# Optimization experiments

Hardware: AMD Instinct MI355X
Metric: run time of the kernel (lower is better)

Reference implementation:

```python
import jax, jax.numpy as jnp
import numpy as np

B, S, H = 8, 4096, 2048
E, F, K = 32, 128, 2
UTIL_BONUS = 0.1
CAP_PENALTY = 0.1


def setup_inputs() -> dict:
    key = jax.random.key(0)
    ks = jax.random.split(key, 4)
    hidden = jax.random.normal(ks[0], (B, S, H), dtype=jnp.float32)
    router_w = 0.02 * jax.random.normal(ks[1], (E, H), dtype=jnp.float32)
    router_b = jnp.zeros((E,), dtype=jnp.float32)
    w1 = 0.02 * jax.random.normal(ks[2], (E, F, H), dtype=jnp.float32)
    b1 = jnp.zeros((E, F), dtype=jnp.float32)
    w2 = 0.02 * jax.random.normal(ks[3], (E, H, F), dtype=jnp.float32)
    b2 = jnp.zeros((E, H), dtype=jnp.float32)
    activation_counts = jnp.zeros((E,), dtype=jnp.float32)
    expert_drift = jnp.zeros((E,), dtype=jnp.float32)
    return {"hidden": hidden, "router_w": router_w, "router_b": router_b,
            "w1": w1, "b1": b1, "w2": w2, "b2": b2,
            "activation_counts": activation_counts, "expert_drift": expert_drift}


def reference(hidden, router_w, router_b, w1, b1, w2, b2, activation_counts, expert_drift):
    # --- router with usage bonus / capacity penalty (buffers are zero at init) ---
    pooled = hidden.mean(axis=1)                      # [B, H]
    base_logits = pooled @ router_w.T + router_b      # [B, E]
    total = activation_counts.sum()
    usage = activation_counts / jnp.maximum(total, 1e-8)
    bonus = jnp.where(total > 0.0, UTIL_BONUS * (1.0 - usage), jnp.zeros_like(usage))
    usage_norm = activation_counts / jnp.maximum(activation_counts.max(), 1e-8)
    drift_norm = expert_drift / jnp.maximum(expert_drift.max(), 1e-8)
    penalty = CAP_PENALTY * 0.5 * (usage_norm + drift_norm)
    logits = base_logits + bonus[None, :] - penalty[None, :]
    router_probs = jax.nn.softmax(logits, axis=-1)    # [B, E]

    topk_probs, topk_idx = jax.lax.top_k(router_probs, K)  # [B, K]
    topk_probs = topk_probs / jnp.maximum(topk_probs.sum(axis=-1, keepdims=True), 1e-8)

    # --- gather selected expert weights and apply to the full sequence ---
    W1 = w1[topk_idx]   # [B, K, F, H]
    B1 = b1[topk_idx]   # [B, K, F]
    W2 = w2[topk_idx]   # [B, K, H, F]
    B2 = b2[topk_idx]   # [B, K, H]

    h1 = jnp.einsum('bsh,bkfh->bksf', hidden, W1) + B1[:, :, None, :]
    h1 = jax.nn.gelu(h1, approximate=False)           # torch nn.GELU default = exact erf
    out = jnp.einsum('bksf,bkhf->bksh', h1, W2) + B2[:, :, None, :]
    delta = jnp.einsum('bk,bksh->bsh', topk_probs, out)  # weighted combine
    return delta, topk_idx, topk_probs, router_probs
```

## Files before the change

### kernel.cpp

```cpp
#include <hip/hip_runtime.h>
#include <hip/hip_bf16.h>

#define BB 8
#define SS 4096
#define HH 2048
#define EE 32
#define FF 128

constexpr size_t DELTA_N = (size_t)BB * SS * HH;
constexpr size_t WELEM = (size_t)EE * FF * HH;
constexpr size_t WBYTES = WELEM * 2;
constexpr size_t HB16_BYTES = (size_t)BB * SS * HH * 2;

typedef short bf16x8 __attribute__((ext_vector_type(8)));
typedef float f32x4 __attribute__((ext_vector_type(4)));
typedef unsigned short u16;
typedef __attribute__((address_space(3))) unsigned char as3u8;
typedef __attribute__((address_space(1))) const unsigned char as1u8;

#define WAITV(N)                                             \
  do {                                                       \
    asm volatile("s_waitcnt vmcnt(" #N ")" ::: "memory");    \
    __builtin_amdgcn_sched_barrier(0);                       \
  } while (0)
#define BARRIER()                                            \
  do {                                                       \
    __builtin_amdgcn_s_barrier();                            \
    __builtin_amdgcn_sched_barrier(0);                       \
  } while (0)

__device__ __forceinline__ u16 f2bfu(float x) {
  unsigned int u = __float_as_uint(x);
  u = (u + 0x7FFFu + ((u >> 16) & 1u)) >> 16;
  return (u16)u;
}

__device__ __forceinline__ unsigned int pk2(float a, float b) {
  union { __hip_bfloat162 h; unsigned int u; } c;
  c.h = __float22bfloat162_rn(make_float2(a, b));
  return c.u;
}

__device__ __forceinline__ bf16x8 pack8(float4 a, float4 b) {
  union { bf16x8 v; unsigned int u[4]; } r;
  r.u[0] = pk2(a.x, a.y);
  r.u[1] = pk2(a.z, a.w);
  r.u[2] = pk2(b.x, b.y);
  r.u[3] = pk2(b.z, b.w);
  return r.v;
}

__device__ __forceinline__ void glds16(const void* g, void* l) {
  __builtin_amdgcn_global_load_lds((as1u8*)g, (as3u8*)l, 16, 0, 0);
}

__global__ void k_zero(float* __restrict__ ws, int n) {
  int i = blockIdx.x * 256 + threadIdx.x;
  if (i < n) ws[i] = 0.0f;
}

__global__ __launch_bounds__(512) void k_poolpack(
    const float* __restrict__ hidden, const float* __restrict__ w1,
    const float* __restrict__ w2, u16* __restrict__ hb16,
    float* __restrict__ psum, u16* __restrict__ w1p, u16* __restrict__ w2p) {
  const int bid = blockIdx.x;
  const int t = threadIdx.x;
  if (bid < 512) {
    const int b  = bid >> 6;
    const int st = bid & 63;
    const float* src = hidden + ((size_t)b * SS + st * 64) * HH + t * 4;
    char* dbase = (char*)hb16 + (size_t)(b * 64 + st) * 262144 + (size_t)(t >> 4) * 8192;
    const int kq = (t & 15) * 8;
    float4 s = make_float4(0.f, 0.f, 0.f, 0.f);
    for (int r = 0; r < 64; ++r) {
      float4 v = *(const float4*)(src + (size_t)r * HH);
      s.x += v.x; s.y += v.y; s.z += v.z; s.w += v.w;
      *(uint2*)(dbase + r * 128 + (kq ^ ((r & 7) << 4))) =
          make_uint2(pk2(v.x, v.y), pk2(v.z, v.w));
    }
    float* pp = psum + (size_t)b * HH + t * 4;
    atomicAdd(pp + 0, s.x);
    atomicAdd(pp + 1, s.y);
    atomicAdd(pp + 2, s.z);
    atomicAdd(pp + 3, s.w);
  } else {
    const int pb = bid - 512;
#pragma unroll 1
    for (int i = 0; i < 8; ++i) {
      unsigned c = (unsigned)pb * 4096u + (unsigned)i * 512u + (unsigned)t;
      const float* src;
      u16* dst;
      if (c < 1048576u) {
        unsigned e = c >> 15, ci = c & 32767u;
        unsigned it = ci >> 10;
        unsigned cb = (ci & 1023u) * 16u;
        unsigned col = cb >> 7;
        unsigned kb = (cb & 127u) ^ ((col & 7u) << 4);
        unsigned k = it * 64u + (kb >> 1);
        src = w1 + ((size_t)(e * 128u + col) * HH + k);
        dst = w1p + (size_t)c * 8;
      } else {
        unsigned c2 = c - 1048576u;
        unsigned e = c2 >> 15, ci = c2 & 32767u;
        unsigned h = ci >> 4;
        unsigned cb = (ci & 15u) * 16u;
        unsigned kb = cb ^ ((h & 7u) << 4);
        unsigned f = kb >> 1;
        src = w2 + ((size_t)(e * 2048u + h) * FF + f);
        dst = w2p + (size_t)c2 * 8;
      }
      float4 a = *(const float4*)src;
      float4 b2v = *(const float4*)(src + 4);
      *(bf16x8*)dst = pack8(a, b2v);
    }
  }
}

__global__ void k_logits(const float* __restrict__ psum, const float* __restrict__ rw,
                         float* __restrict__ logits) {
  int b = blockIdx.x >> 5;
  int e = blockIdx.x & 31;
  int tid = threadIdx.x;
  float acc = 0.0f;
  const float* ps = psum + (size_t)b * HH;
  const float* wr = rw + (size_t)e * HH;
  for (int h = tid; h < HH; h += 256) acc = fmaf(ps[h], wr[h], acc);
  __shared__ float red[256];
  red[tid] = acc;
  __syncthreads();
  for (int w = 128; w > 0; w >>= 1) {
    if (tid < w) red[tid] += red[tid + w];
    __syncthreads();
  }
  if (tid == 0) logits[blockIdx.x] = red[0] * (1.0f / (float)SS);
}

__global__ void k_topk(const float* __restrict__ logits, const float* __restrict__ rb,
                       const float* __restrict__ counts, const float* __restrict__ drift,
                       int* __restrict__ sel, float* __restrict__ pscale,
                       float* __restrict__ out) {
  int t = threadIdx.x;
  int b = t >> 5, e = t & 31;
  float total = 0.0f, cmax = 0.0f, dmax = 0.0f;
  for (int i = 0; i < EE; ++i) {
    float c = counts[i]; total += c; cmax = fmaxf(cmax, c);
    float d = drift[i];  dmax = fmaxf(dmax, d);
  }
  float cnt = counts[e], dr = drift[e];
  float usage = cnt / fmaxf(total, 1e-8f);
  float bonus = (total > 0.0f) ? 0.1f * (1.0f - usage) : 0.0f;
  float un = cnt / fmaxf(cmax, 1e-8f);
  float dn = dr / fmaxf(dmax, 1e-8f);
  float l = logits[t] + rb[e] + bonus - 0.05f * (un + dn);

  float m = l;
  for (int w = 16; w; w >>= 1) m = fmaxf(m, __shfl_xor(m, w, 32));
  float p = expf(l - m);
  float ssum = p;
  for (int w = 16; w; w >>= 1) ssum += __shfl_xor(ssum, w, 32);
  float prob = p / ssum;
  out[DELTA_N + 32 + t] = prob;

  float v1 = prob; int i1 = e;
  for (int w = 16; w; w >>= 1) {
    float ov = __shfl_xor(v1, w, 32); int oi = __shfl_xor(i1, w, 32);
    if (ov > v1 || (ov == v1 && oi < i1)) { v1 = ov; i1 = oi; }
  }
  float v2 = (e == i1) ? -1.0f : prob; int i2 = e;
  for (int w = 16; w; w >>= 1) {
    float ov = __shfl_xor(v2, w, 32); int oi = __shfl_xor(i2, w, 32);
    if (ov > v2 || (ov == v2 && oi < i2)) { v2 = ov; i2 = oi; }
  }
  if (e == 0) {
    float denom = fmaxf(v1 + v2, 1e-8f);
    float tp0 = v1 / denom, tp1 = v2 / denom;
    sel[b * 2 + 0] = i1;
    sel[b * 2 + 1] = i2;
    pscale[b * 2 + 0] = tp0;
    pscale[b * 2 + 1] = tp1;
    out[DELTA_N + 0 + b * 2 + 0] = (float)i1;
    out[DELTA_N + 0 + b * 2 + 1] = (float)i2;
    out[DELTA_N + 16 + b * 2 + 0] = tp0;
    out[DELTA_N + 16 + b * 2 + 1] = tp1;
  }
}

__global__ __launch_bounds__(512, 4) void k_ffn5(
    const u16* __restrict__ hb16, const float* __restrict__ bs1,
    const float* __restrict__ bs2, const u16* __restrict__ w1p,
    const u16* __restrict__ w2p, const int* __restrict__ sel,
    const float* __restrict__ pscale, float* __restrict__ out) {
  __shared__ __align__(16) char smem[81920];

  const int t    = threadIdx.x;
  const int lane = t & 63;
  const int wv   = t >> 6;
  const int l15  = lane & 15;
  const int lk   = lane >> 4;

  const int bid = blockIdx.x;
  const int b   = bid & 7;
  const int st  = bid >> 3;

  const int e0 = sel[2 * b], e1 = sel[2 * b + 1];
  const float p0 = pscale[2 * b], p1 = pscale[2 * b + 1];

  const int wr = wv >> 2, wc = wv & 3;
  const int RB = wr * 32, CB = wc * 64;

  const char* hsrc = (const char*)hb16 + (size_t)(b * 64 + st) * 262144 + (size_t)t * 16;
  const size_t eB1 = (size_t)((wv < 4) ? e0 : e1) * 524288;
  const char* bsrc = (const char*)w1p + eB1 + (size_t)(wv & 3) * 4096 + (size_t)lane * 16;

  f32x4 zero = {0.f, 0.f, 0.f, 0.f};
  f32x4 acc1[2][4];
#pragma unroll
  for (int i = 0; i < 2; ++i)
#pragma unroll
    for (int j = 0; j < 4; ++j) acc1[i][j] = zero;

  auto STAGE1 = [&](int bb, int j) {
    glds16(hsrc + (size_t)j * 8192, &smem[65536 + bb * 8192 + (size_t)t * 16]);
    const char* s = bsrc + (size_t)j * 16384;
    char* d = &smem[bb * 32768 + wv * 4096 + lane * 16];
#pragma unroll
    for (int r = 0; r < 4; ++r) glds16(s + r * 1024, d + r * 1024);
  };

  STAGE1(0, 0);
  STAGE1(1, 1);

#pragma unroll 1
  for (int j = 0; j < 32; ++j) {
    if (j < 31) { WAITV(5); } else { WAITV(0); }
    BARRIER();
    const int cb = j & 1;
    const char* sa = &smem[65536 + cb * 8192];
    const char* sb = &smem[cb * 32768];
#pragma unroll
    for (int kk = 0; kk < 2; ++kk) {
      bf16x8 af[2], bv[4];
#pragma unroll
      for (int rt = 0; rt < 2; ++rt) {
        int row = RB + rt * 16 + l15;
        af[rt] = *(const bf16x8*)(sa + row * 128 + ((kk * 64 + lk * 16) ^ ((row & 7) << 4)));
      }
#pragma unroll
      for (int ct = 0; ct < 4; ++ct) {
        int col = CB + ct * 16 + l15;
        bv[ct] = *(const bf16x8*)(sb + col * 128 + ((kk * 64 + lk * 16) ^ ((col & 7) << 4)));
      }
#pragma unroll
      for (int rt = 0; rt < 2; ++rt)
#pragma unroll
        for (int ct = 0; ct < 4; ++ct)
          acc1[rt][ct] = __builtin_amdgcn_mfma_f32_16x16x32_bf16(af[rt], bv[ct], acc1[rt][ct], 0, 0, 0);
    }
    BARRIER();
    if (j < 30) STAGE1(j & 1, j + 2);
  }

#pragma unroll
  for (int ct = 0; ct < 4; ++ct) {
    int c = CB + ct * 16 + l15;
    int ec = (c < 128) ? e0 : e1;
    float pc = (c < 128) ? p0 : p1;
    float bias = bs1[ec * FF + (c & 127)];
#pragma unroll
    for (int rt = 0; rt < 2; ++rt)
#pragma unroll
      for (int r = 0; r < 4; ++r) {
        int row = RB + rt * 16 + lk * 4 + r;
        float x = acc1[rt][ct][r] + bias;
        float g = 0.5f * x * (1.0f + erff(x * 0.70710678118654752f));
        *(u16*)&smem[row * 512 + ((c * 2) ^ ((row & 7) << 4))] = f2bfu(pc * g);
      }
  }
  {
    float4 q0 = *(const float4*)(bs2 + (size_t)e0 * HH + t * 4);
    float4 q1 = *(const float4*)(bs2 + (size_t)e1 * HH + t * 4);
    float4 bb;
    bb.x = p0 * q0.x + p1 * q1.x;
    bb.y = p0 * q0.y + p1 * q1.y;
    bb.z = p0 * q0.z + p1 * q1.z;
    bb.w = p0 * q0.w + p1 * q1.w;
    *(float4*)&smem[65536 + t * 16] = bb;
  }
  __syncthreads();

  const int wr2 = wv >> 2, wc2 = wv & 3;
  bf16x8 pa[2][8];
#pragma unroll
  for (int rt = 0; rt < 2; ++rt) {
    int row = wr2 * 32 + rt * 16 + l15;
    unsigned sw = (row & 7) << 4;
#pragma unroll
    for (int ks = 0; ks < 8; ++ks)
      pa[rt][ks] = *(const bf16x8*)&smem[row * 512 + ((ks * 64 + lk * 16) ^ sw)];
  }
  BARRIER();

  const char* wse = (const char*)w2p + (size_t)((wv < 4) ? e0 : e1) * 524288;
  auto STAGE2 = [&](int bb, int n) {
    const char* s = wse + (size_t)(n * 64 + (wv & 3) * 16) * 256 + (size_t)lane * 16;
    char* d = &smem[bb * 32768 + (wv >> 2) * 16384 + (wv & 3) * 4096 + lane * 16];
#pragma unroll
    for (int i = 0; i < 4; ++i) glds16(s + i * 1024, d + i * 1024);
  };
  STAGE2(0, 0);
  STAGE2(1, 1);

  float* obase = out + ((size_t)b * SS + st * 64) * HH;
  const int h64 = wc2 * 16 + l15;

#pragma unroll 1
  for (int n0 = 0; n0 < 32; ++n0) {
    if (n0 == 0) { WAITV(4); }
    else if (n0 == 31) { WAITV(8); }
    else { WAITV(12); }
    BARRIER();
    const char* tb = &smem[(n0 & 1) * 32768];
    float bias = *(const float*)&smem[65536 + (n0 * 64 + h64) * 4];
    f32x4 acc2[2];
    acc2[0] = zero; acc2[1] = zero;
#pragma unroll
    for (int ks = 0; ks < 8; ++ks) {
      bf16x8 bv = *(const bf16x8*)(tb + (ks >> 2) * 16384 + h64 * 256 +
                                   (((ks & 3) * 64 + lk * 16) ^ ((h64 & 7) << 4)));
#pragma unroll
      for (int rt = 0; rt < 2; ++rt)
        acc2[rt] = __builtin_amdgcn_mfma_f32_16x16x32_bf16(pa[rt][ks], bv, acc2[rt], 0, 0, 0);
    }
    BARRIER();
    const int col = n0 * 64 + h64;
#pragma unroll
    for (int rt = 0; rt < 2; ++rt)
#pragma unroll
      for (int r = 0; r < 4; ++r) {
        int row = wr2 * 32 + rt * 16 + lk * 4 + r;
        obase[(size_t)row * HH + col] = acc2[rt][r] + bias;
      }
    if (n0 < 30) STAGE2(n0 & 1, n0 + 2);
  }
}

__global__ void k_pool_logits(const float* __restrict__ hidden,
                              const float* __restrict__ rw,
                              float* __restrict__ logits) {
  const int b  = blockIdx.x >> 6;
  const int hc = (blockIdx.x >> 3) & 7;
  const int sq = blockIdx.x & 7;
  const int t  = threadIdx.x;
  const int tx = t & 63;
  const int qq = t >> 6;
  const int h0 = hc * 256;

  const float* p = hidden + ((size_t)b * SS + sq * 512 + qq * 128) * HH + h0 + tx * 4;
  float4 s = make_float4(0.f, 0.f, 0.f, 0.f);
  for (int i = 0; i < 128; ++i) {
    float4 v = *(const float4*)(p + (size_t)i * HH);
    s.x += v.x; s.y += v.y; s.z += v.z; s.w += v.w;
  }
  __shared__ float ps[4][256];
  __shared__ float pl[256];
  *(float4*)&ps[qq][tx * 4] = s;
  __syncthreads();
  pl[t] = ps[0][t] + ps[1][t] + ps[2][t] + ps[3][t];
  __syncthreads();

  const int e = t >> 3, part = t & 7;
  const float* wrp = rw + (size_t)e * HH + h0 + part * 32;
  float v = 0.f;
#pragma unroll
  for (int m = 0; m < 32; ++m) v += pl[part * 32 + m] * wrp[m];
  v += __shfl_xor(v, 1, 8);
  v += __shfl_xor(v, 2, 8);
  v += __shfl_xor(v, 4, 8);
  if (part == 0) atomicAdd(&logits[b * EE + e], v * (1.0f / (float)SS));
}

__global__ __launch_bounds__(512, 2) void k_ffn_fb(
    const float* __restrict__ hidden, const float* __restrict__ w1,
    const float* __restrict__ b1, const float* __restrict__ w2,
    const float* __restrict__ b2, const int* __restrict__ sel,
    const float* __restrict__ pscale, float* __restrict__ out) {
  __shared__ unsigned char sA[2][64 * 128];
  __shared__ unsigned char sG[64 * 512];

  const int t    = threadIdx.x;
  const int lane = t & 63;
  const int wv   = t >> 6;
  const int wr   = wv >> 2;
  const int wc   = wv & 3;
  const int l15  = lane & 15;
  const int lk   = lane >> 4;

  const int bid = blockIdx.x;
  const int b   = bid & 7;
  const int s0  = (bid >> 3) * 64;

  const int e0 = sel[2 * b], e1 = sel[2 * b + 1];
  const float p0 = pscale[2 * b], p1 = pscale[2 * b + 1];

  const float* hbase = hidden + ((size_t)b * SS + s0) * HH;
  const int srow = t >> 4;
  const int skq  = t & 15;

  float4 R[2];
  const float* wp[4];
#pragma unroll
  for (int ct = 0; ct < 4; ++ct) {
    int cbase = wc * 64 + ct * 16;
    int ec = (cbase < 128) ? e0 : e1;
    int f  = (cbase & 127) + l15;
    wp[ct] = w1 + ((size_t)ec * FF + f) * HH + lk * 8;
  }

  f32x4 zero = {0.f, 0.f, 0.f, 0.f};
  f32x4 acc1[2][4];
#pragma unroll
  for (int i = 0; i < 2; ++i)
#pragma unroll
    for (int j = 0; j < 4; ++j) acc1[i][j] = zero;

#pragma unroll
  for (int p = 0; p < 2; ++p)
    R[p] = *(const float4*)(hbase + (size_t)(srow + 32 * p) * HH + skq * 4);
#pragma unroll
  for (int p = 0; p < 2; ++p) {
    int row = srow + 32 * p;
    int addr = row * 128 + ((skq * 8) ^ ((row & 7) << 4));
    *(uint2*)(&sA[0][addr]) = make_uint2(pk2(R[p].x, R[p].y), pk2(R[p].z, R[p].w));
  }
  __syncthreads();

  for (int it = 0; it < 32; ++it) {
    const int buf = it & 1;
    if (it < 31) {
      const int k0 = (it + 1) * 64;
#pragma unroll
      for (int p = 0; p < 2; ++p)
        R[p] = *(const float4*)(hbase + (size_t)(srow + 32 * p) * HH + k0 + skq * 4);
    }
#pragma unroll
    for (int kk = 0; kk < 2; ++kk) {
      bf16x8 a[2];
#pragma unroll
      for (int rt = 0; rt < 2; ++rt) {
        int row = wr * 32 + rt * 16 + l15;
        a[rt] = *(const bf16x8*)(&sA[buf][row * 128 + ((kk * 64 + lk * 16) ^ ((row & 7) << 4))]);
      }
#pragma unroll
      for (int ct = 0; ct < 4; ++ct) {
        const float* q = wp[ct] + it * 64 + kk * 32;
        bf16x8 bfr = pack8(*(const float4*)q, *(const float4*)(q + 4));
#pragma unroll
        for (int rt = 0; rt < 2; ++rt)
          acc1[rt][ct] = __builtin_amdgcn_mfma_f32_16x16x32_bf16(a[rt], bfr, acc1[rt][ct], 0, 0, 0);
      }
    }
    if (it < 31) {
#pragma unroll
      for (int p = 0; p < 2; ++p) {
        int row = srow + 32 * p;
        int addr = row * 128 + ((skq * 8) ^ ((row & 7) << 4));
        *(uint2*)(&sA[buf ^ 1][addr]) = make_uint2(pk2(R[p].x, R[p].y), pk2(R[p].z, R[p].w));
      }
    }
    __syncthreads();
  }

#pragma unroll
  for (int ct = 0; ct < 4; ++ct) {
    int c = wc * 64 + ct * 16 + l15;
    int ec = (c < 128) ? e0 : e1;
    float pc = (c < 128) ? p0 : p1;
    float bias = b1[ec * FF + (c & 127)];
#pragma unroll
    for (int rt = 0; rt < 2; ++rt)
#pragma unroll
      for (int r = 0; r < 4; ++r) {
        int row = wr * 32 + rt * 16 + lk * 4 + r;
        float x = acc1[rt][ct][r] + bias;
        float g = 0.5f * x * (1.0f + erff(x * 0.70710678118654752f));
        int addr = row * 512 + ((c * 2) ^ ((row & 7) << 4));
        *(u16*)(&sG[addr]) = f2bfu(pc * g);
      }
  }
  __syncthreads();

  bf16x8 pa[2][8];
#pragma unroll
  for (int rt = 0; rt < 2; ++rt) {
    int row = wr * 32 + rt * 16 + l15;
#pragma unroll
    for (int ks = 0; ks < 8; ++ks)
      pa[rt][ks] = *(const bf16x8*)(&sG[row * 512 + ((ks * 64 + lk * 16) ^ ((row & 7) << 4))]);
  }

  float* obase = out + ((size_t)b * SS + s0) * HH;
  for (int ct = 0; ct < 32; ++ct) {
    const int h = wc * 512 + ct * 16 + l15;
    f32x4 acc[2];
    acc[0] = zero; acc[1] = zero;
    const float* q0 = w2 + ((size_t)e0 * HH + h) * FF + lk * 8;
    const float* q1 = w2 + ((size_t)e1 * HH + h) * FF + lk * 8;
#pragma unroll
    for (int ks = 0; ks < 8; ++ks) {
      const float* q = (ks < 4 ? q0 : q1) + (ks & 3) * 32;
      bf16x8 bfr = pack8(*(const float4*)q, *(const float4*)(q + 4));
#pragma unroll
      for (int rt = 0; rt < 2; ++rt)
        acc[rt] = __builtin_amdgcn_mfma_f32_16x16x32_bf16(pa[rt][ks], bfr, acc[rt], 0, 0, 0);
    }
    float bias = p0 * b2[(size_t)e0 * HH + h] + p1 * b2[(size_t)e1 * HH + h];
#pragma unroll
    for (int rt = 0; rt < 2; ++rt)
#pragma unroll
      for (int r = 0; r < 4; ++r) {
        int row = wr * 32 + rt * 16 + lk * 4 + r;
        obase[(size_t)row * HH + h] = acc[rt][r] + bias;
      }
  }
}

extern "C" void kernel_launch(void* const* d_in, const int* in_sizes, int n_in,
                              void* d_out, int out_size, void* d_ws, size_t ws_size,
                              hipStream_t stream) {
  const float* hidden   = (const float*)d_in[0];
  const float* router_w = (const float*)d_in[1];
  const float* router_b = (const float*)d_in[2];
  const float* w1       = (const float*)d_in[3];
  const float* b1       = (const float*)d_in[4];
  const float* w2       = (const float*)d_in[5];
  const float* b2       = (const float*)d_in[6];
  const float* counts   = (const float*)d_in[7];
  const float* drift    = (const float*)d_in[8];
  float* out            = (float*)d_out;

  float* logits = (float*)d_ws;
  int*   sel    = (int*)((char*)d_ws + 1024);
  float* pscale = (float*)((char*)d_ws + 1088);
  float* psum   = (float*)((char*)d_ws + 4096);

  const size_t need_big = 131072 + 2 * WBYTES + HB16_BYTES;

  if (ws_size >= need_big) {
    u16* w1p  = (u16*)((char*)d_ws + 131072);
    u16* w2p  = (u16*)((char*)d_ws + 131072 + WBYTES);
    u16* hb16 = (u16*)((char*)d_ws + 131072 + 2 * WBYTES);
    k_zero<<<68, 256, 0, stream>>>(logits, 17408);
    k_poolpack<<<1024, 512, 0, stream>>>(hidden, w1, w2, hb16, psum, w1p, w2p);
    k_logits<<<256, 256, 0, stream>>>(psum, router_w, logits);
    k_topk<<<1, 256, 0, stream>>>(logits, router_b, counts, drift, sel, pscale, out);
    k_ffn5<<<512, 512, 0, stream>>>(hb16, b1, b2, w1p, w2p, sel, pscale, out);
  } else {
    k_zero<<<2, 256, 0, stream>>>(logits, 288);
    k_pool_logits<<<512, 256, 0, stream>>>(hidden, router_w, logits);
    k_topk<<<1, 256, 0, stream>>>(logits, router_b, counts, drift, sel, pscale, out);
    k_ffn_fb<<<512, 512, 0, stream>>>(hidden, w1, b1, w2, b2, sel, pscale, out);
  }
}
```

Measured before the change: 260.9 us.

## Drop bf16 hidden copy; convert fp32 activations in-kernel via register prefetch

The pooling kernel no longer writes a bf16 packed copy of the hidden tensor. The FFN kernel now loads fp32 hidden rows into registers one k-step ahead, converts them to bf16 and writes them into a single swizzled LDS A-buffer, while weights keep using direct global-to-LDS loads. This removes a full-size intermediate write and re-read, at the cost of reading twice the bytes of activation data inside the FFN kernel and adding register pressure and lgkm waits. s_setprio is also raised around the MFMA sections.

```diff
diff --git a/kernel.cpp b/kernel.cpp
--- a/kernel.cpp
+++ b/kernel.cpp
@@ -10,7 +10,6 @@
 constexpr size_t DELTA_N = (size_t)BB * SS * HH;
 constexpr size_t WELEM = (size_t)EE * FF * HH;
 constexpr size_t WBYTES = WELEM * 2;
-constexpr size_t HB16_BYTES = (size_t)BB * SS * HH * 2;
 
 typedef short bf16x8 __attribute__((ext_vector_type(8)));
 typedef float f32x4 __attribute__((ext_vector_type(4)));
@@ -21,6 +20,11 @@
 #define WAITV(N)                                             \
   do {                                                       \
     asm volatile("s_waitcnt vmcnt(" #N ")" ::: "memory");    \
+    __builtin_amdgcn_sched_barrier(0);                       \
+  } while (0)
+#define WAITLGKM()                                           \
+  do {                                                       \
+    asm volatile("s_waitcnt lgkmcnt(0)" ::: "memory");       \
     __builtin_amdgcn_sched_barrier(0);                       \
   } while (0)
 #define BARRIER()                                            \
@@ -61,22 +65,18 @@
 
 __global__ __launch_bounds__(512) void k_poolpack(
     const float* __restrict__ hidden, const float* __restrict__ w1,
-    const float* __restrict__ w2, u16* __restrict__ hb16,
-    float* __restrict__ psum, u16* __restrict__ w1p, u16* __restrict__ w2p) {
+    const float* __restrict__ w2, float* __restrict__ psum,
+    u16* __restrict__ w1p, u16* __restrict__ w2p) {
   const int bid = blockIdx.x;
   const int t = threadIdx.x;
   if (bid < 512) {
     const int b  = bid >> 6;
     const int st = bid & 63;
     const float* src = hidden + ((size_t)b * SS + st * 64) * HH + t * 4;
-    char* dbase = (char*)hb16 + (size_t)(b * 64 + st) * 262144 + (size_t)(t >> 4) * 8192;
-    const int kq = (t & 15) * 8;
     float4 s = make_float4(0.f, 0.f, 0.f, 0.f);
     for (int r = 0; r < 64; ++r) {
       float4 v = *(const float4*)(src + (size_t)r * HH);
       s.x += v.x; s.y += v.y; s.z += v.z; s.w += v.w;
-      *(uint2*)(dbase + r * 128 + (kq ^ ((r & 7) << 4))) =
-          make_uint2(pk2(v.x, v.y), pk2(v.z, v.w));
     }
     float* pp = psum + (size_t)b * HH + t * 4;
     atomicAdd(pp + 0, s.x);
@@ -185,8 +185,8 @@
   }
 }
 
-__global__ __launch_bounds__(512, 4) void k_ffn5(
-    const u16* __restrict__ hb16, const float* __restrict__ bs1,
+__global__ __launch_bounds__(512, 4) void k_ffn6(
+    const float* __restrict__ hidden, const float* __restrict__ bs1,
     const float* __restrict__ bs2, const u16* __restrict__ w1p,
     const u16* __restrict__ w2p, const int* __restrict__ sel,
     const float* __restrict__ pscale, float* __restrict__ out) {
@@ -208,7 +208,10 @@
   const int wr = wv >> 2, wc = wv & 3;
   const int RB = wr * 32, CB = wc * 64;
 
-  const char* hsrc = (const char*)hb16 + (size_t)(b * 64 + st) * 262144 + (size_t)t * 16;
+  const int srow = t >> 4;
+  const int skq  = t & 15;
+  const float* hbase = hidden + ((size_t)b * SS + st * 64) * HH;
+
   const size_t eB1 = (size_t)((wv < 4) ? e0 : e1) * 524288;
   const char* bsrc = (const char*)w1p + eB1 + (size_t)(wv & 3) * 4096 + (size_t)lane * 16;
 
@@ -219,31 +222,49 @@
 #pragma unroll
     for (int j = 0; j < 4; ++j) acc1[i][j] = zero;
 
-  auto STAGE1 = [&](int bb, int j) {
-    glds16(hsrc + (size_t)j * 8192, &smem[65536 + bb * 8192 + (size_t)t * 16]);
+  float4 RA0, RA1;
+  auto LOADA = [&](int j) {
+    RA0 = *(const float4*)(hbase + (size_t)srow * HH + j * 64 + skq * 4);
+    RA1 = *(const float4*)(hbase + (size_t)(srow + 32) * HH + j * 64 + skq * 4);
+  };
+  auto WRITEA = [&]() {
+    int a0 = 65536 + srow * 128 + ((skq * 8) ^ ((srow & 7) << 4));
+    int r1 = srow + 32;
+    int a1 = 65536 + r1 * 128 + ((skq * 8) ^ ((r1 & 7) << 4));
+    *(uint2*)&smem[a0] = make_uint2(pk2(RA0.x, RA0.y), pk2(RA0.z, RA0.w));
+    *(uint2*)&smem[a1] = make_uint2(pk2(RA1.x, RA1.y), pk2(RA1.z, RA1.w));
+  };
+  auto STAGEB = [&](int bb, int j) {
     const char* s = bsrc + (size_t)j * 16384;
     char* d = &smem[bb * 32768 + wv * 4096 + lane * 16];
 #pragma unroll
     for (int r = 0; r < 4; ++r) glds16(s + r * 1024, d + r * 1024);
   };
 
-  STAGE1(0, 0);
-  STAGE1(1, 1);
+  STAGEB(0, 0);
+  __builtin_amdgcn_sched_barrier(0);
+  LOADA(0);
+  __builtin_amdgcn_sched_barrier(0);
+  STAGEB(1, 1);
+  WAITV(4);
+  WRITEA();
 
 #pragma unroll 1
   for (int j = 0; j < 32; ++j) {
-    if (j < 31) { WAITV(5); } else { WAITV(0); }
+    WAITLGKM();
     BARRIER();
-    const int cb = j & 1;
-    const char* sa = &smem[65536 + cb * 8192];
-    const char* sb = &smem[cb * 32768];
+    if (j < 31) LOADA(j + 1);
+    __builtin_amdgcn_sched_barrier(0);
+    const char* sb = &smem[(j & 1) * 32768];
+    __builtin_amdgcn_s_setprio(1);
 #pragma unroll
     for (int kk = 0; kk < 2; ++kk) {
       bf16x8 af[2], bv[4];
 #pragma unroll
       for (int rt = 0; rt < 2; ++rt) {
         int row = RB + rt * 16 + l15;
-        af[rt] = *(const bf16x8*)(sa + row * 128 + ((kk * 64 + lk * 16) ^ ((row & 7) << 4)));
+        af[rt] = *(const bf16x8*)(&smem[65536 + row * 128 +
+                                        ((kk * 64 + lk * 16) ^ ((row & 7) << 4))]);
       }
 #pragma unroll
       for (int ct = 0; ct < 4; ++ct) {
@@ -256,8 +277,13 @@
         for (int ct = 0; ct < 4; ++ct)
           acc1[rt][ct] = __builtin_amdgcn_mfma_f32_16x16x32_bf16(af[rt], bv[ct], acc1[rt][ct], 0, 0, 0);
     }
+    __builtin_amdgcn_s_setprio(0);
     BARRIER();
-    if (j < 30) STAGE1(j & 1, j + 2);
+    if (j < 31) {
+      if (j < 30) { STAGEB(j & 1, j + 2); WAITV(4); }
+      else        { WAITV(0); }
+      WRITEA();
+    }
   }
 
 #pragma unroll
@@ -284,7 +310,7 @@
     bb.y = p0 * q0.y + p1 * q1.y;
     bb.z = p0 * q0.z + p1 * q1.z;
     bb.w = p0 * q0.w + p1 * q1.w;
-    *(float4*)&smem[65536 + t * 16] = bb;
+    *(float4*)&smem[73728 + t * 16] = bb;
   }
   __syncthreads();
 
@@ -298,6 +324,7 @@
     for (int ks = 0; ks < 8; ++ks)
       pa[rt][ks] = *(const bf16x8*)&smem[row * 512 + ((ks * 64 + lk * 16) ^ sw)];
   }
+  WAITLGKM();
   BARRIER();
 
   const char* wse = (const char*)w2p + (size_t)((wv < 4) ? e0 : e1) * 524288;
@@ -320,9 +347,10 @@
     else { WAITV(12); }
     BARRIER();
     const char* tb = &smem[(n0 & 1) * 32768];
-    float bias = *(const float*)&smem[65536 + (n0 * 64 + h64) * 4];
+    float bias = *(const float*)&smem[73728 + (n0 * 64 + h64) * 4];
     f32x4 acc2[2];
     acc2[0] = zero; acc2[1] = zero;
+    __builtin_amdgcn_s_setprio(1);
 #pragma unroll
     for (int ks = 0; ks < 8; ++ks) {
       bf16x8 bv = *(const bf16x8*)(tb + (ks >> 2) * 16384 + h64 * 256 +
@@ -331,6 +359,7 @@
       for (int rt = 0; rt < 2; ++rt)
         acc2[rt] = __builtin_amdgcn_mfma_f32_16x16x32_bf16(pa[rt][ks], bv, acc2[rt], 0, 0, 0);
     }
+    __builtin_amdgcn_s_setprio(0);
     BARRIER();
     const int col = n0 * 64 + h64;
 #pragma unroll
@@ -543,17 +572,16 @@
   float* pscale = (float*)((char*)d_ws + 1088);
   float* psum   = (float*)((char*)d_ws + 4096);
 
-  const size_t need_big = 131072 + 2 * WBYTES + HB16_BYTES;
+  const size_t need_big = 131072 + 2 * WBYTES + 64;
 
   if (ws_size >= need_big) {
-    u16* w1p  = (u16*)((char*)d_ws + 131072);
-    u16* w2p  = (u16*)((char*)d_ws + 131072 + WBYTES);
-    u16* hb16 = (u16*)((char*)d_ws + 131072 + 2 * WBYTES);
+    u16* w1p = (u16*)((char*)d_ws + 131072);
+    u16* w2p = (u16*)((char*)d_ws + 131072 + WBYTES);
     k_zero<<<68, 256, 0, stream>>>(logits, 17408);
-    k_poolpack<<<1024, 512, 0, stream>>>(hidden, w1, w2, hb16, psum, w1p, w2p);
+    k_poolpack<<<1024, 512, 0, stream>>>(hidden, w1, w2, psum, w1p, w2p);
     k_logits<<<256, 256, 0, stream>>>(psum, router_w, logits);
     k_topk<<<1, 256, 0, stream>>>(logits, router_b, counts, drift, sel, pscale, out);
-    k_ffn5<<<512, 512, 0, stream>>>(hb16, b1, b2, w1p, w2p, sel, pscale, out);
+    k_ffn6<<<512, 512, 0, stream>>>(hidden, b1, b2, w1p, w2p, sel, pscale, out);
   } else {
     k_zero<<<2, 256, 0, stream>>>(logits, 288);
     k_pool_logits<<<512, 256, 0, stream>>>(hidden, router_w, logits);
```

New measurement: 286.2 us. 9.7% more time.
